# Performance work log

Measured on AMD Instinct MI355X. Metric: run time of the kernel, lower is better.

Reference implementation:

```python
import jax, jax.numpy as jnp
import numpy as np

N_NODES = 100000
N_EDGES = 1600000


def setup_inputs() -> dict:
    key = jax.random.key(0)
    k1, k2, k3, k4, k5 = jax.random.split(key, 5)
    node_states = jax.random.normal(k1, (N_NODES, 128), dtype=jnp.float32)
    edge_index = jax.random.randint(k2, (2, N_EDGES), 0, N_NODES, dtype=jnp.int64)
    mask = jax.random.uniform(k3, (N_EDGES,), dtype=jnp.float32)  # edge weights
    # Glorot-ish init for the two GCN linear layers
    W1 = jax.random.normal(k4, (128, 64), dtype=jnp.float32) * 0.05
    b1 = jnp.zeros((64,), dtype=jnp.float32)
    W2 = jax.random.normal(k5, (64, 64), dtype=jnp.float32) * 0.05
    b2 = jnp.zeros((64,), dtype=jnp.float32)
    return {"node_states": node_states, "edge_index": edge_index, "mask": mask,
            "W1": W1, "b1": b1, "W2": W2, "b2": b2}


def _gcn_layer(x, src, dst, edge_w, W, b, n_nodes):
    # PyG GCNConv (normalize=False): h = x @ W; out[dst] += edge_w * h[src]; out += b
    h = x @ W                                  # [N, d_out]
    msg = h[src] * edge_w[:, None]             # [E, d_out] gather + scale
    agg = jax.ops.segment_sum(msg, dst, num_segments=n_nodes)  # scatter-add
    return agg + b


def reference(node_states, edge_index, mask, W1, b1, W2, b2):
    src = edge_index[0]
    dst = edge_index[1]
    n = node_states.shape[0]
    h1 = jax.nn.relu(_gcn_layer(node_states, src, dst, mask, W1, b1, n))
    h2 = jax.nn.relu(_gcn_layer(h1, src, dst, mask, W2, b2, n))
    return h2
```

## Files before the change

### kernel.cpp

```cpp
#include <hip/hip_runtime.h>
#include <hip/hip_bf16.h>

#define N_NODES 100000
#define N_EDGES 1600000
#define NBUCKET 1563
#define NBLK_S 391
#define CHUNK_E 4096
#define CAP 1280
#define GCSTRIDE 32
#define FIXSCALE 1048576.0f
#define FIXINV   (1.0f / 1048576.0f)

typedef short v8s __attribute__((ext_vector_type(8)));
typedef float v4f __attribute__((ext_vector_type(4)));

static __device__ __forceinline__ unsigned pack_bf2(float a, float b) {
    __hip_bfloat162 p = __float22bfloat162_rn(make_float2(a, b));
    return *reinterpret_cast<unsigned*>(&p);
}
static __device__ __forceinline__ float2 bf2_to_f2(unsigned u) {
    __hip_bfloat162 p = *reinterpret_cast<__hip_bfloat162*>(&u);
    return __bfloat1622float2(p);
}

__global__ __launch_bounds__(1024) void k1_sort_gemm(const int* __restrict__ src,
                                                     const int* __restrict__ dst,
                                                     const float* __restrict__ wgt,
                                                     const float* __restrict__ x,
                                                     const float* __restrict__ W1,
                                                     int* __restrict__ gcount,
                                                     int2* __restrict__ arena,
                                                     unsigned* __restrict__ hpre) {
    __shared__ __align__(16) int smem[18004];
    const int b = blockIdx.x;
    const int t = threadIdx.x;

    if (b >= NBLK_S) {
        unsigned* xs = (unsigned*)smem;
        unsigned* ws = (unsigned*)smem + 64 * 68;
        const int tile = b - NBLK_S;
        const int row0 = tile * 64;
        {
            const float2* g2 = (const float2*)W1;
            for (int i = t; i < 64 * 128 / 2; i += 1024) {
                const float2 v = g2[i];
                const int k = (2 * i) >> 6;
                const int c = (2 * i) & 63;
                ((short*)&ws[c * 68])[k]       = (short)(pack_bf2(v.x, 0.f) & 0xFFFF);
                ((short*)&ws[(c + 1) * 68])[k] = (short)(pack_bf2(v.y, 0.f) & 0xFFFF);
            }
        }
        {
            const float4* g = (const float4*)x;
            for (int i = t; i < 64 * 32; i += 1024) {
                const int r = i >> 5, cu = i & 31;
                const int row = row0 + r;
                uint2 v = make_uint2(0u, 0u);
                if (row < N_NODES) {
                    float4 f = g[(size_t)row * 32 + cu];
                    v.x = pack_bf2(f.x, f.y);
                    v.y = pack_bf2(f.z, f.w);
                }
                *(uint2*)&xs[r * 68 + 2 * cu] = v;
            }
        }
        __syncthreads();
        const int w = t >> 6, lane = t & 63;
        const int l15 = lane & 15, quad = lane >> 4;
        const int a  = w & 3;
        const int g_ = w >> 2;
        v4f acc = (v4f){0.f, 0.f, 0.f, 0.f};
#pragma unroll
        for (int k0 = 0; k0 < 128; k0 += 32) {
            const int ku = k0 / 2 + quad * 4;
            const v8s xb = *(const v8s*)&xs[(g_ * 16 + l15) * 68 + ku];
            const v8s wa = *(const v8s*)&ws[(16 * a + l15) * 68 + ku];
            acc = __builtin_amdgcn_mfma_f32_16x16x32_bf16(wa, xb, acc, 0, 0, 0);
        }
        const int node = row0 + g_ * 16 + l15;
        if (node < N_NODES) {
            uint2 o;
            o.x = pack_bf2(acc[0], acc[1]);
            o.y = pack_bf2(acc[2], acc[3]);
            *(uint2*)&hpre[(size_t)node * 32 + 8 * a + 2 * quad] = o;
        }
        return;
    }

    int*  hist  = smem;
    int*  lcur  = smem + 1563;
    int*  tgb   = smem + 3126;
    int*  pairs = smem + 4689;
    int*  tg    = smem + 5713;
    int2* ord   = (int2*)(smem + 9810);

    for (int i = t; i < NBUCKET; i += 1024) hist[i] = 0;
    __syncthreads();

    const int e0 = b * CHUNK_E;
    const int n = min(CHUNK_E, N_EDGES - e0);
    const int nI4 = n >> 2;
    const bool act = t < nI4;
    int4 sv, dv; float4 wv;
    if (act) {
        sv = ((const int4*)(src + e0))[t];
        dv = ((const int4*)(dst + e0))[t];
        wv = ((const float4*)(wgt + e0))[t];
        atomicAdd(&hist[dv.x >> 6], 1);
        atomicAdd(&hist[dv.y >> 6], 1);
        atomicAdd(&hist[dv.z >> 6], 1);
        atomicAdd(&hist[dv.w >> 6], 1);
    }
    __syncthreads();
    {
        int a0 = 0, a1 = 0;
        if (2 * t < NBUCKET) a0 = hist[2 * t];
        if (2 * t + 1 < NBUCKET) a1 = hist[2 * t + 1];
        pairs[t] = a0 + a1;
    }
    __syncthreads();
    for (int off = 1; off < 1024; off <<= 1) {
        const int u = (t >= off) ? pairs[t - off] : 0;
        __syncthreads();
        pairs[t] += u;
        __syncthreads();
    }
    if (2 * t < NBUCKET) {
        const int a0 = hist[2 * t];
        const int a1 = (2 * t + 1 < NBUCKET) ? hist[2 * t + 1] : 0;
        const int incl = pairs[t];
        lcur[2 * t] = incl - a0 - a1;
        if (2 * t + 1 < NBUCKET) lcur[2 * t + 1] = incl - a1;
    }
    __syncthreads();
    for (int i = t; i < NBUCKET; i += 1024) {
        const int hv = hist[i];
        const int lb = lcur[i];
        const int grsv = (hv > 0) ? atomicAdd(&gcount[i * GCSTRIDE], hv) : 0;
        tgb[i] = i * CAP + grsv - lb;
    }
    __syncthreads();
    if (act) {
        {
            const int bk = dv.x >> 6;
            const int lp = atomicAdd(&lcur[bk], 1);
            ord[lp] = make_int2(sv.x | ((dv.x & 63) << 17), __float_as_int(wv.x));
            tg[lp] = tgb[bk] + lp;
        }
        {
            const int bk = dv.y >> 6;
            const int lp = atomicAdd(&lcur[bk], 1);
            ord[lp] = make_int2(sv.y | ((dv.y & 63) << 17), __float_as_int(wv.y));
            tg[lp] = tgb[bk] + lp;
        }
        {
            const int bk = dv.z >> 6;
            const int lp = atomicAdd(&lcur[bk], 1);
            ord[lp] = make_int2(sv.z | ((dv.z & 63) << 17), __float_as_int(wv.z));
            tg[lp] = tgb[bk] + lp;
        }
        {
            const int bk = dv.w >> 6;
            const int lp = atomicAdd(&lcur[bk], 1);
            ord[lp] = make_int2(sv.w | ((dv.w & 63) << 17), __float_as_int(wv.w));
            tg[lp] = tgb[bk] + lp;
        }
    }
    __syncthreads();
    for (int i = t; i < n; i += 1024)
        arena[tg[i]] = ord[i];
}

static __device__ __forceinline__ void acc_rec(int* __restrict__ accs, int2 r,
                                               unsigned hv, int li) {
    const int dl = (r.x >> 17) & 63;
    const float wt = __int_as_float(r.y);
    const float2 f = bf2_to_f2(hv);
    atomicAdd(&accs[dl * 64 + 2 * li],     (int)(wt * f.x * FIXSCALE));
    atomicAdd(&accs[dl * 64 + 2 * li + 1], (int)(wt * f.y * FIXSCALE));
}

template<bool FUSE>
__global__ __launch_bounds__(256) void gather_fuse(const unsigned* __restrict__ hsrc,
                                                   const int2* __restrict__ arena,
                                                   const int* __restrict__ gcount,
                                                   const float* __restrict__ bias,
                                                   const float* __restrict__ W2,
                                                   void* __restrict__ outp) {
    __shared__ int accs[64 * 64];
    extern __shared__ unsigned wsdyn[];
    const int b = blockIdx.x;
    const int t = threadIdx.x;
    for (int i = t; i < 4096; i += 256) accs[i] = 0;
    if constexpr (FUSE) {
        const float2* g2 = (const float2*)W2;
        for (int i = t; i < 2048; i += 256) {
            const float2 v = g2[i];
            const int k = (2 * i) >> 6;
            const int c = (2 * i) & 63;
            ((short*)&wsdyn[c * 36])[k]       = (short)(pack_bf2(v.x, 0.f) & 0xFFFF);
            ((short*)&wsdyn[(c + 1) * 36])[k] = (short)(pack_bf2(v.y, 0.f) & 0xFFFF);
        }
    }
    __syncthreads();
    const int cnt = gcount[b * GCSTRIDE];
    const size_t base = (size_t)b * CAP;
    const int lane = t & 63;
    const int li = lane & 31;
    int i = (t >> 6) * 2 + (lane >> 5);
    for (; i + 24 < cnt; i += 32) {
        const int2 r0 = arena[base + i];
        const int2 r1 = arena[base + i + 8];
        const int2 r2 = arena[base + i + 16];
        const int2 r3 = arena[base + i + 24];
        const unsigned h0 = hsrc[(size_t)(r0.x & 0x1FFFF) * 32 + li];
        const unsigned h1 = hsrc[(size_t)(r1.x & 0x1FFFF) * 32 + li];
        const unsigned h2 = hsrc[(size_t)(r2.x & 0x1FFFF) * 32 + li];
        const unsigned h3 = hsrc[(size_t)(r3.x & 0x1FFFF) * 32 + li];
        acc_rec(accs, r0, h0, li);
        acc_rec(accs, r1, h1, li);
        acc_rec(accs, r2, h2, li);
        acc_rec(accs, r3, h3, li);
    }
    for (; i < cnt; i += 8) {
        const int2 r = arena[base + i];
        const unsigned h = hsrc[(size_t)(r.x & 0x1FFFF) * 32 + li];
        acc_rec(accs, r, h, li);
    }
    __syncthreads();

    if constexpr (FUSE) {
        unsigned pk[8];
#pragma unroll
        for (int k = 0; k < 8; ++k) {
            const int i2 = t + k * 256;
            const int node = i2 >> 5, cp = i2 & 31;
            const float f0 = fmaxf((float)accs[node * 64 + 2 * cp]     * FIXINV + bias[2 * cp],     0.f);
            const float f1 = fmaxf((float)accs[node * 64 + 2 * cp + 1] * FIXINV + bias[2 * cp + 1], 0.f);
            pk[k] = pack_bf2(f0, f1);
        }
        __syncthreads();
        unsigned* xs = (unsigned*)accs;
#pragma unroll
        for (int k = 0; k < 8; ++k) {
            const int i2 = t + k * 256;
            const int node = i2 >> 5, cp = i2 & 31;
            xs[node * 36 + cp] = pk[k];
        }
        __syncthreads();
        const int w = t >> 6, l15 = lane & 15, quad = lane >> 4;
        v4f a4[4];
#pragma unroll
        for (int tt = 0; tt < 4; ++tt) a4[tt] = (v4f){0.f, 0.f, 0.f, 0.f};
#pragma unroll
        for (int k0 = 0; k0 < 64; k0 += 32) {
            const int ku = k0 / 2 + quad * 4;
            const v8s xb = *(const v8s*)&xs[(w * 16 + l15) * 36 + ku];
#pragma unroll
            for (int tt = 0; tt < 4; ++tt) {
                const v8s wa = *(const v8s*)&wsdyn[(16 * tt + l15) * 36 + ku];
                a4[tt] = __builtin_amdgcn_mfma_f32_16x16x32_bf16(wa, xb, a4[tt], 0, 0, 0);
            }
        }
        const int ng = b * 64 + w * 16 + l15;
        if (ng < N_NODES) {
#pragma unroll
            for (int tt = 0; tt < 4; ++tt) {
                uint2 o;
                o.x = pack_bf2(a4[tt][0], a4[tt][1]);
                o.y = pack_bf2(a4[tt][2], a4[tt][3]);
                *(uint2*)&((unsigned*)outp)[(size_t)ng * 32 + 8 * tt + 2 * quad] = o;
            }
        }
    } else {
        for (int i2 = t; i2 < 2048; i2 += 256) {
            const int node = i2 >> 5, cp = i2 & 31;
            const int ng = b * 64 + node;
            if (ng < N_NODES) {
                float2 o;
                o.x = fmaxf((float)accs[node * 64 + 2 * cp]     * FIXINV + bias[2 * cp],     0.f);
                o.y = fmaxf((float)accs[node * 64 + 2 * cp + 1] * FIXINV + bias[2 * cp + 1], 0.f);
                *(float2*)&((float*)outp)[(size_t)ng * 64 + 2 * cp] = o;
            }
        }
    }
}

extern "C" void kernel_launch(void* const* d_in, const int* in_sizes, int n_in,
                              void* d_out, int out_size, void* d_ws, size_t ws_size,
                              hipStream_t stream) {
    const float* x    = (const float*)d_in[0];
    const int*   eidx = (const int*)d_in[1];
    const float* mask = (const float*)d_in[2];
    const float* W1   = (const float*)d_in[3];
    const float* b1   = (const float*)d_in[4];
    const float* W2   = (const float*)d_in[5];
    const float* b2   = (const float*)d_in[6];
    float* out = (float*)d_out;

    const int* src = eidx;
    const int* dst = eidx + N_EDGES;

    unsigned* hpre = (unsigned*)d_out;

    int2*     arena  = (int2*)d_ws;
    int*      gcount = (int*)(arena + (size_t)NBUCKET * CAP);
    unsigned* hpre2  = (unsigned*)(gcount + NBUCKET * GCSTRIDE);

    const int gemmBlocks = (N_NODES + 63) / 64;

    hipMemsetAsync(gcount, 0, NBUCKET * GCSTRIDE * sizeof(int), stream);

    k1_sort_gemm<<<NBLK_S + gemmBlocks, 1024, 0, stream>>>(src, dst, mask, x, W1,
                                                           gcount, arena, hpre);

    gather_fuse<true><<<NBUCKET, 256, 64 * 36 * 4, stream>>>(hpre, arena, gcount,
                                                             b1, W2, hpre2);
    gather_fuse<false><<<NBUCKET, 256, 0, stream>>>(hpre2, arena, gcount,
                                                    b2, nullptr, out);
}
```

Baseline: 255.5 us.

## Repack hidden features as (d, d+32) pairs with LDS-staged coalesced stores

Each packed bf16 word of the hidden features now holds feature d and feature d+32 rather than two adjacent features. Because of this, the scatter-add atomics into shared memory hit consecutive words per lane (li and 32+li) instead of a stride-2 pattern, which is meant to reduce LDS bank conflicts. The MFMA outputs of both GEMMs are staged through padded shared memory so the global stores become contiguous per thread. The gather loop is also unrolled to eight records to keep more loads in flight, at the cost of extra syncs and more registers.

```diff
diff --git a/kernel.cpp b/kernel.cpp
--- a/kernel.cpp
+++ b/kernel.cpp
@@ -10,6 +10,7 @@
 #define GCSTRIDE 32
 #define FIXSCALE 1048576.0f
 #define FIXINV   (1.0f / 1048576.0f)
+
 
 typedef short v8s __attribute__((ext_vector_type(8)));
 typedef float v4f __attribute__((ext_vector_type(4)));
@@ -77,12 +78,15 @@
             const v8s wa = *(const v8s*)&ws[(16 * a + l15) * 68 + ku];
             acc = __builtin_amdgcn_mfma_f32_16x16x32_bf16(wa, xb, acc, 0, 0, 0);
         }
-        const int node = row0 + g_ * 16 + l15;
-        if (node < N_NODES) {
-            uint2 o;
-            o.x = pack_bf2(acc[0], acc[1]);
-            o.y = pack_bf2(acc[2], acc[3]);
-            *(uint2*)&hpre[(size_t)node * 32 + 8 * a + 2 * quad] = o;
+        __syncthreads();
+        float* stg = (float*)smem;
+        *(v4f*)&stg[(g_ * 16 + l15) * 68 + 16 * a + 4 * quad] = acc;
+        __syncthreads();
+        for (int i2 = t; i2 < 2048; i2 += 1024) {
+            const int nl = i2 >> 5, d = i2 & 31;
+            const int row = row0 + nl;
+            if (row < N_NODES)
+                hpre[(size_t)row * 32 + d] = pack_bf2(stg[nl * 68 + d], stg[nl * 68 + d + 32]);
         }
         return;
     }
@@ -174,10 +178,10 @@
 static __device__ __forceinline__ void acc_rec(int* __restrict__ accs, int2 r,
                                                unsigned hv, int li) {
     const int dl = (r.x >> 17) & 63;
-    const float wt = __int_as_float(r.y);
+    const float ws = __int_as_float(r.y) * FIXSCALE;
     const float2 f = bf2_to_f2(hv);
-    atomicAdd(&accs[dl * 64 + 2 * li],     (int)(wt * f.x * FIXSCALE));
-    atomicAdd(&accs[dl * 64 + 2 * li + 1], (int)(wt * f.y * FIXSCALE));
+    atomicAdd(&accs[dl * 64 + li],      (int)(ws * f.x));
+    atomicAdd(&accs[dl * 64 + 32 + li], (int)(ws * f.y));
 }
 
 template<bool FUSE>
@@ -187,7 +191,7 @@
                                                    const float* __restrict__ bias,
                                                    const float* __restrict__ W2,
                                                    void* __restrict__ outp) {
-    __shared__ int accs[64 * 64];
+    __shared__ int accs[64 * 68];
     extern __shared__ unsigned wsdyn[];
     const int b = blockIdx.x;
     const int t = threadIdx.x;
@@ -208,19 +212,31 @@
     const int lane = t & 63;
     const int li = lane & 31;
     int i = (t >> 6) * 2 + (lane >> 5);
-    for (; i + 24 < cnt; i += 32) {
-        const int2 r0 = arena[base + i];
-        const int2 r1 = arena[base + i + 8];
-        const int2 r2 = arena[base + i + 16];
-        const int2 r3 = arena[base + i + 24];
-        const unsigned h0 = hsrc[(size_t)(r0.x & 0x1FFFF) * 32 + li];
-        const unsigned h1 = hsrc[(size_t)(r1.x & 0x1FFFF) * 32 + li];
-        const unsigned h2 = hsrc[(size_t)(r2.x & 0x1FFFF) * 32 + li];
-        const unsigned h3 = hsrc[(size_t)(r3.x & 0x1FFFF) * 32 + li];
+    for (; i + 56 < cnt; i += 64) {
+        int2 r0 = arena[base + i];
+        int2 r1 = arena[base + i + 8];
+        int2 r2 = arena[base + i + 16];
+        int2 r3 = arena[base + i + 24];
+        int2 r4 = arena[base + i + 32];
+        int2 r5 = arena[base + i + 40];
+        int2 r6 = arena[base + i + 48];
+        int2 r7 = arena[base + i + 56];
+        unsigned h0 = hsrc[(size_t)(r0.x & 0x1FFFF) * 32 + li];
+        unsigned h1 = hsrc[(size_t)(r1.x & 0x1FFFF) * 32 + li];
+        unsigned h2 = hsrc[(size_t)(r2.x & 0x1FFFF) * 32 + li];
+        unsigned h3 = hsrc[(size_t)(r3.x & 0x1FFFF) * 32 + li];
+        unsigned h4 = hsrc[(size_t)(r4.x & 0x1FFFF) * 32 + li];
+        unsigned h5 = hsrc[(size_t)(r5.x & 0x1FFFF) * 32 + li];
+        unsigned h6 = hsrc[(size_t)(r6.x & 0x1FFFF) * 32 + li];
+        unsigned h7 = hsrc[(size_t)(r7.x & 0x1FFFF) * 32 + li];
         acc_rec(accs, r0, h0, li);
         acc_rec(accs, r1, h1, li);
         acc_rec(accs, r2, h2, li);
         acc_rec(accs, r3, h3, li);
+        acc_rec(accs, r4, h4, li);
+        acc_rec(accs, r5, h5, li);
+        acc_rec(accs, r6, h6, li);
+        acc_rec(accs, r7, h7, li);
     }
     for (; i < cnt; i += 8) {
         const int2 r = arena[base + i];
@@ -262,15 +278,18 @@
                 a4[tt] = __builtin_amdgcn_mfma_f32_16x16x32_bf16(wa, xb, a4[tt], 0, 0, 0);
             }
         }
-        const int ng = b * 64 + w * 16 + l15;
-        if (ng < N_NODES) {
-#pragma unroll
-            for (int tt = 0; tt < 4; ++tt) {
-                uint2 o;
-                o.x = pack_bf2(a4[tt][0], a4[tt][1]);
-                o.y = pack_bf2(a4[tt][2], a4[tt][3]);
-                *(uint2*)&((unsigned*)outp)[(size_t)ng * 32 + 8 * tt + 2 * quad] = o;
-            }
+        __syncthreads();
+        float* stg = (float*)accs;
+#pragma unroll
+        for (int tt = 0; tt < 4; ++tt)
+            *(v4f*)&stg[(w * 16 + l15) * 68 + 16 * tt + 4 * quad] = a4[tt];
+        __syncthreads();
+        for (int i2 = t; i2 < 2048; i2 += 256) {
+            const int nl = i2 >> 5, d = i2 & 31;
+            const int ng = b * 64 + nl;
+            if (ng < N_NODES)
+                ((unsigned*)outp)[(size_t)ng * 32 + d] =
+                    pack_bf2(stg[nl * 68 + d], stg[nl * 68 + d + 32]);
         }
     } else {
         for (int i2 = t; i2 < 2048; i2 += 256) {
```

New measurement: 245.0 us. 1.04x faster.
